# Kernel optimization log

Hardware: AMD Instinct MI355X
Metric: run time of the kernel (lower is better)

Reference implementation:

```python
import jax, jax.numpy as jnp
from jax import lax
import numpy as np

TAG_NAMES = ["O", "B-MAT", "I-MAT", "B-PRO", "I-PRO", "B-APL", "I-APL", "B-SMT", "I-SMT", "B-CMT", "I-CMT", "B-DSC", "I-DSC"]
IMP = -100.0


def _init_crf_params(key):
    # torchcrf initializes uniform(-0.1, 0.1); CRF_NEW then clamps invalid
    # BIO transitions to -100 per define_invalid_crf_transitions/init_crf_transitions.
    K = len(TAG_NAMES)
    k1, k2, k3 = jax.random.split(key, 3)
    start = np.array(jax.random.uniform(k1, (K,), minval=-0.1, maxval=0.1), dtype=np.float32)
    end = np.array(jax.random.uniform(k2, (K,), minval=-0.1, maxval=0.1), dtype=np.float32)
    trans = np.array(jax.random.uniform(k3, (K, K), minval=-0.1, maxval=0.1), dtype=np.float32)
    pref = [t[0] for t in TAG_NAMES]
    ent = [t.split('-')[1] if '-' in t else '' for t in TAG_NAMES]
    for i in range(K):
        if pref[i] in ('B', 'I'):  # invalid begin/end for BIO
            start[i] = IMP
            end[i] = IMP
    for i in range(K):
        for j in range(K):
            # invalid_transitions_position: O -> I  (B->P, I->P are empty sets)
            if pref[i] == 'O' and pref[j] == 'I':
                trans[i, j] = IMP
            # invalid_transitions_tags: B->I, I->I across different entity types
            if pref[i] in ('B', 'I') and pref[j] == 'I' and ent[i] != ent[j]:
                trans[i, j] = IMP
    return jnp.asarray(start), jnp.asarray(end), jnp.asarray(trans)


def setup_inputs() -> dict:
    key = jax.random.key(0)
    k_em, k_tag, k_p = jax.random.split(key, 3)
    B, T, K = 4096, 512, len(TAG_NAMES)
    emissions = jax.random.normal(k_em, (B, T, K), dtype=jnp.float32)
    tags = jax.random.randint(k_tag, (B, T), 0, K, dtype=jnp.int64)
    mask = jnp.ones((B, T), dtype=bool)
    start_transitions, end_transitions, transitions = _init_crf_params(k_p)
    return {"emissions": emissions, "tags": tags, "mask": mask,
            "start_transitions": start_transitions,
            "end_transitions": end_transitions,
            "transitions": transitions}


def reference(emissions, tags, mask, start_transitions, end_transitions, transitions):
    # torchcrf CRF.forward with batch_first=True, reduction='sum':
    # returns sum over batch of log p(tags | emissions).
    B, T, K = emissions.shape
    maskf = mask.astype(emissions.dtype)

    # ---- numerator: score of the given tag path ----
    emit = jnp.take_along_axis(emissions, tags[..., None], axis=2)[..., 0]  # [B,T]
    trans = transitions[tags[:, :-1], tags[:, 1:]]                           # [B,T-1]
    num = start_transitions[tags[:, 0]] + emit[:, 0]
    num = num + jnp.sum((trans + emit[:, 1:]) * maskf[:, 1:], axis=1)
    seq_ends = jnp.sum(mask.astype(jnp.int32), axis=1) - 1                   # [B]
    last_tags = tags[jnp.arange(B), seq_ends]
    num = num + end_transitions[last_tags]

    # ---- denominator: log partition via forward-algorithm scan over time ----
    em_t = jnp.swapaxes(emissions, 0, 1)   # [T,B,K]
    mask_t = jnp.swapaxes(mask, 0, 1)      # [T,B]
    score0 = start_transitions + em_t[0]   # [B,K]

    def step(score, xs):
        em, m = xs  # em: [B,K], m: [B]
        # broadcast: [B,K_from,1] + [K_from,K_to] + [B,1,K_to]
        nxt = jax.nn.logsumexp(score[:, :, None] + transitions[None] + em[:, None, :], axis=1)
        return jnp.where(m[:, None], nxt, score), None

    score, _ = lax.scan(step, score0, (em_t[1:], mask_t[1:]))
    denom = jax.nn.logsumexp(score + end_transitions, axis=1)  # [B]

    return jnp.sum(num - denom)
```

## Files before the change

### kernel.cpp

```cpp
#include <hip/hip_runtime.h>


typedef float  f4  __attribute__((ext_vector_type(4)));
typedef float  f4u __attribute__((ext_vector_type(4), aligned(4)));
typedef int    i4  __attribute__((ext_vector_type(4)));
typedef __bf16 bh8 __attribute__((ext_vector_type(8)));

#define FENCE do { __builtin_amdgcn_sched_barrier(0); \
                   asm volatile("" ::: "memory"); } while (0)

__device__ __forceinline__ unsigned pack_bf16(float x, float y) {
  return __builtin_amdgcn_perm(__float_as_uint(y) + 0x8000u,
                               __float_as_uint(x) + 0x8000u, 0x07060302u);
}

__global__ void __launch_bounds__(192, 1)
crf_main(const float* __restrict__ em,
         const int*   __restrict__ tags,
         const float* __restrict__ startT,
         const float* __restrict__ endT,
         const float* __restrict__ trans,
         float* __restrict__ partial)
{
  __shared__ float ldsT[256];
  __shared__ float ldsS[16], ldsE[16];
  __shared__ float pFa[256];
  __shared__ float lsF[16], numF[16], resB[16];

  const int tid = threadIdx.x;
  for (int i = tid; i < 169; i += 192) {
    const int r_ = i / 13, c_ = i - r_ * 13;
    ldsT[r_ * 16 + c_] = trans[i];
  }
  if (tid < 13) ldsS[tid] = startT[tid];
  if (tid >= 16 && tid < 29) ldsE[tid - 16] = endT[tid - 16];
  __syncthreads();

  const int lane = tid & 63;
  const int wv   = tid >> 6;
  const int n    = lane & 15;
  const int q    = lane >> 4;

  f4  D = {0.f, 0.f, 0.f, 0.f};
  int ls2 = 0;
  float sDs0 = 0, sDs1 = 0, sDs2 = 0, sDs3 = 0;

  if (wv == 2) {
    const int s = q;
    const int seq = blockIdx.x * 16 + n;
    const int* tq = tags + (size_t)seq * 512;
    const float* emQ = em + (size_t)seq * 6656;
    const int t0base = 128 * s;
    float nacc = 0.0f;
    int prev = (s > 0) ? tq[t0base - 1] : 0;
#pragma unroll 4
    for (int g = 0; g < 32; ++g) {
      const int t0 = t0base + 4 * g;
      const int4 tv = *(const int4*)(tq + t0);
      nacc += emQ[(size_t)(t0 + 0) * 13 + tv.x];
      nacc += emQ[(size_t)(t0 + 1) * 13 + tv.y];
      nacc += emQ[(size_t)(t0 + 2) * 13 + tv.z];
      nacc += emQ[(size_t)(t0 + 3) * 13 + tv.w];
      if (!(s == 0 && g == 0)) nacc += ldsT[prev * 16 + tv.x];
      nacc += ldsT[tv.x * 16 + tv.y] + ldsT[tv.y * 16 + tv.z]
            + ldsT[tv.z * 16 + tv.w];
      prev = tv.w;
    }
    if (s == 0) nacc += ldsS[tq[0]];
    if (s == 3) nacc += ldsE[prev];
    nacc += __shfl_xor(nacc, 16, 64);
    nacc += __shfl_xor(nacc, 32, 64);
    if (s == 0) numF[n] = nacc;
  } else {
    const bool is_fwd = (wv == 0);
    const int seq = blockIdx.x * 16 + n;
    const int loadBase = (q < 3) ? 4 * q : 9;
    const float* emP = em + (size_t)seq * 6656 + loadBase;

    bh8 afrag;
    {
      float av[4];
#pragma unroll
      for (int i = 0; i < 4; ++i) {
        const int kk = 4 * q + i;
        av[i] = (kk < 13 && n < 13)
              ? __expf(is_fwd ? ldsT[kk * 16 + n] : ldsT[n * 16 + kk]) : 0.0f;
      }
      i4 ai = { (int)pack_bf16(av[0], av[1]), (int)pack_bf16(av[2], av[3]), 0, 0 };
      afrag = __builtin_bit_cast(bh8, ai);
    }

#pragma unroll
    for (int r = 0; r < 4; ++r) {
      const int m = 4 * q + r;
      D[r] = (m < 13) ? __expf(is_fwd ? ldsS[m] : ldsE[m]) : 0.0f;
    }

    int   epend = 0;
    float rcCur = 1.0f;
    f4 eA[16], eB[16];

#define LOADE(EB, TC) do {                                              \
    const int tc_ = (TC);                                               \
    _Pragma("unroll")                                                   \
    for (int k_ = 0; k_ < 16; ++k_)                                     \
      EB[k_] = *(const f4u*)(emP + (size_t)(tc_ + k_) * 13);            \
  } while (0)

#define RNMEAS() do {                                                   \
    float cm_ = fmaxf(fmaxf(Ds0, Ds1), fmaxf(Ds2, Ds3));                \
    cm_ = fmaxf(cm_, __shfl_xor(cm_, 16, 64));                          \
    cm_ = fmaxf(cm_, __shfl_xor(cm_, 32, 64));                          \
    const int eb_ = (int)(__float_as_uint(cm_) >> 23);                  \
    epend = eb_ - 126;                                                  \
    rcCur = __uint_as_float((unsigned)(253 - eb_) << 23);               \
  } while (0)

#define CORE(EM4, KPH) do {                                             \
    float e0 = __expf((q == 3) ? (EM4).w : (EM4).x);                    \
    float e1 = __expf((EM4).y);                                         \
    float e2 = __expf((EM4).z);                                         \
    float e3 = __expf((EM4).w);                                         \
    if ((KPH) == 7) { e0 *= rcCur; e1 *= rcCur; e2 *= rcCur; e3 *= rcCur; \
                      ls2 += epend; }                                   \
    Ds0 = D[0] * e0; Ds1 = D[1] * e1; Ds2 = D[2] * e2; Ds3 = D[3] * e3; \
    if ((KPH) == 5) RNMEAS();                                           \
    {                                                                   \
      i4 bi_ = { (int)pack_bf16(Ds0, Ds1), (int)pack_bf16(Ds2, Ds3), 0, 0 }; \
      bh8 bf_ = __builtin_bit_cast(bh8, bi_);                           \
      D = __builtin_amdgcn_mfma_f32_16x16x32_bf16(                      \
              afrag, bf_, (f4){0.f, 0.f, 0.f, 0.f}, 0, 0, 0);           \
    }                                                                   \
  } while (0)

#define PROCF(EB, LAST) do {                                            \
    _Pragma("unroll")                                                   \
    for (int k = 0; k < 16; ++k) {                                      \
      const f4 em4 = EB[k];                                             \
      float Ds0, Ds1, Ds2, Ds3;                                         \
      CORE(em4, (k & 7));                                               \
      if ((LAST) && k == 15) { sDs0 = Ds0; sDs1 = Ds1; sDs2 = Ds2; sDs3 = Ds3; } \
    }                                                                   \
  } while (0)

#define PROCB(EB) do {                                                  \
    _Pragma("unroll")                                                   \
    for (int kk = 0; kk < 16; ++kk) {                                   \
      const f4 em4 = EB[15 - kk];                                       \
      float Ds0, Ds1, Ds2, Ds3;                                         \
      CORE(em4, (kk & 7));                                              \
    }                                                                   \
  } while (0)

    if (is_fwd) {
      LOADE(eA, 0); LOADE(eB, 16); FENCE;
      PROCF(eA, false);
      for (int it = 0; it < 7; ++it) {
        LOADE(eA, 32 * it + 32); FENCE;
        PROCF(eB, false);
        LOADE(eB, 32 * it + 48); FENCE;
        PROCF(eA, false);
      }
      FENCE;
      PROCF(eB, true);
      if (q == 0) lsF[n] = (float)ls2 * 0.6931471805599453f;
      *(f4*)&pFa[n * 16 + 4 * q] = (f4){sDs0, sDs1, sDs2, sDs3};
    } else {
      LOADE(eA, 496); LOADE(eB, 480); FENCE;
      PROCB(eA);
      for (int it = 0; it < 7; ++it) {
        LOADE(eA, 464 - 32 * it); FENCE;
        PROCB(eB);
        LOADE(eB, 448 - 32 * it); FENCE;
        PROCB(eA);
      }
      FENCE;
      PROCB(eB);
    }
#undef LOADE
#undef RNMEAS
#undef CORE
#undef PROCF
#undef PROCB
  }

  __syncthreads();

  if (wv == 1) {
    const f4 al = *(const f4*)&pFa[n * 16 + 4 * q];
    float z = al[0] * D[0] + al[1] * D[1] + al[2] * D[2] + al[3] * D[3];
    z += __shfl_xor(z, 16, 64);
    z += __shfl_xor(z, 32, 64);
    const float denom = lsF[n] + (float)ls2 * 0.6931471805599453f + __logf(z);
    if (q == 0) resB[n] = numF[n] - denom;
  }
  __syncthreads();
  if (tid == 0) {
    float s = 0.0f;
#pragma unroll
    for (int i = 0; i < 16; ++i) s += resB[i];
    partial[blockIdx.x] = s;
  }
}

__global__ void __launch_bounds__(256)
crf_reduce(const float* __restrict__ part, float* __restrict__ out, int n)
{
  float v = 0.0f;
  for (int i = threadIdx.x; i < n; i += 256) v += part[i];
#pragma unroll
  for (int off = 32; off > 0; off >>= 1) v += __shfl_down(v, off);
  __shared__ float w[4];
  if ((threadIdx.x & 63) == 0) w[threadIdx.x >> 6] = v;
  __syncthreads();
  if (threadIdx.x == 0) out[0] = (w[0] + w[1]) + (w[2] + w[3]);
}

extern "C" void kernel_launch(void* const* d_in, const int* in_sizes, int n_in,
                              void* d_out, int out_size, void* d_ws, size_t ws_size,
                              hipStream_t stream) {
  const float* em   = (const float*)d_in[0];
  const int*   tags = (const int*)d_in[1];
  const float* st   = (const float*)d_in[3];
  const float* en   = (const float*)d_in[4];
  const float* tr   = (const float*)d_in[5];
  float* part = (float*)d_ws;

  crf_main<<<256, 192, 0, stream>>>(em, tags, st, en, tr, part);
  crf_reduce<<<1, 256, 0, stream>>>(part, (float*)d_out, 256);
}
```

Baseline: 190.8 us.

## Split each sequence's scan into eight parallel chunks of transfer-matrix products

Replaces the two-wave forward/backward scan over 16 sequences per block with one wavefront per sequence. Each wavefront builds eight 13x13 transfer-matrix products over separate time chunks in parallel, using bf16 16x16x16 MFMAs with periodic exponent renormalisation, then chains them with shuffles. The numerator moves to separate blocks and the reduction combines per-sequence numerator and denominator arrays. This adds far more parallel work per sequence to hide the serial MFMA latency of the scan, at the cost of more total MFMA work and more bf16 rounding through the matrix products.

```diff
diff --git a/kernel.cpp b/kernel.cpp
--- a/kernel.cpp
+++ b/kernel.cpp
@@ -2,38 +2,33 @@
 
 
 typedef float  f4  __attribute__((ext_vector_type(4)));
-typedef float  f4u __attribute__((ext_vector_type(4), aligned(4)));
-typedef int    i4  __attribute__((ext_vector_type(4)));
-typedef __bf16 bh8 __attribute__((ext_vector_type(8)));
-
-#define FENCE do { __builtin_amdgcn_sched_barrier(0); \
-                   asm volatile("" ::: "memory"); } while (0)
+typedef short  s4  __attribute__((ext_vector_type(4)));
+typedef int    i2  __attribute__((ext_vector_type(2)));
 
 __device__ __forceinline__ unsigned pack_bf16(float x, float y) {
   return __builtin_amdgcn_perm(__float_as_uint(y) + 0x8000u,
                                __float_as_uint(x) + 0x8000u, 0x07060302u);
 }
 
-__global__ void __launch_bounds__(192, 1)
+__global__ void __launch_bounds__(256)
 crf_main(const float* __restrict__ em,
          const int*   __restrict__ tags,
          const float* __restrict__ startT,
          const float* __restrict__ endT,
          const float* __restrict__ trans,
-         float* __restrict__ partial)
+         float* __restrict__ pnum,
+         float* __restrict__ pden)
 {
   __shared__ float ldsT[256];
   __shared__ float ldsS[16], ldsE[16];
-  __shared__ float pFa[256];
-  __shared__ float lsF[16], numF[16], resB[16];
 
   const int tid = threadIdx.x;
-  for (int i = tid; i < 169; i += 192) {
-    const int r_ = i / 13, c_ = i - r_ * 13;
-    ldsT[r_ * 16 + c_] = trans[i];
-  }
-  if (tid < 13) ldsS[tid] = startT[tid];
-  if (tid >= 16 && tid < 29) ldsE[tid - 16] = endT[tid - 16];
+  for (int i = tid; i < 256; i += 256) {
+    const int r_ = i >> 4, c_ = i & 15;
+    ldsT[i] = (r_ < 13 && c_ < 13) ? trans[r_ * 13 + c_] : -100.0f;
+  }
+  if (tid < 16) ldsS[tid] = (tid < 13) ? startT[tid] : -100.0f;
+  if (tid >= 16 && tid < 32) ldsE[tid - 16] = (tid < 29) ? endT[tid - 16] : -100.0f;
   __syncthreads();
 
   const int lane = tid & 63;
@@ -41,13 +36,9 @@
   const int n    = lane & 15;
   const int q    = lane >> 4;
 
-  f4  D = {0.f, 0.f, 0.f, 0.f};
-  int ls2 = 0;
-  float sDs0 = 0, sDs1 = 0, sDs2 = 0, sDs3 = 0;
-
-  if (wv == 2) {
+  if (blockIdx.x < 64) {
     const int s = q;
-    const int seq = blockIdx.x * 16 + n;
+    const int seq = blockIdx.x * 64 + wv * 16 + n;
     const int* tq = tags + (size_t)seq * 512;
     const float* emQ = em + (size_t)seq * 6656;
     const int t0base = 128 * s;
@@ -70,144 +61,123 @@
     if (s == 3) nacc += ldsE[prev];
     nacc += __shfl_xor(nacc, 16, 64);
     nacc += __shfl_xor(nacc, 32, 64);
-    if (s == 0) numF[n] = nacc;
-  } else {
-    const bool is_fwd = (wv == 0);
-    const int seq = blockIdx.x * 16 + n;
-    const int loadBase = (q < 3) ? 4 * q : 9;
-    const float* emP = em + (size_t)seq * 6656 + loadBase;
-
-    bh8 afrag;
-    {
-      float av[4];
-#pragma unroll
-      for (int i = 0; i < 4; ++i) {
-        const int kk = 4 * q + i;
-        av[i] = (kk < 13 && n < 13)
-              ? __expf(is_fwd ? ldsT[kk * 16 + n] : ldsT[n * 16 + kk]) : 0.0f;
-      }
-      i4 ai = { (int)pack_bf16(av[0], av[1]), (int)pack_bf16(av[2], av[3]), 0, 0 };
-      afrag = __builtin_bit_cast(bh8, ai);
-    }
-
-#pragma unroll
-    for (int r = 0; r < 4; ++r) {
-      const int m = 4 * q + r;
-      D[r] = (m < 13) ? __expf(is_fwd ? ldsS[m] : ldsE[m]) : 0.0f;
-    }
-
-    int   epend = 0;
-    float rcCur = 1.0f;
-    f4 eA[16], eB[16];
-
-#define LOADE(EB, TC) do {                                              \
-    const int tc_ = (TC);                                               \
-    _Pragma("unroll")                                                   \
-    for (int k_ = 0; k_ < 16; ++k_)                                     \
-      EB[k_] = *(const f4u*)(emP + (size_t)(tc_ + k_) * 13);            \
-  } while (0)
-
-#define RNMEAS() do {                                                   \
-    float cm_ = fmaxf(fmaxf(Ds0, Ds1), fmaxf(Ds2, Ds3));                \
-    cm_ = fmaxf(cm_, __shfl_xor(cm_, 16, 64));                          \
-    cm_ = fmaxf(cm_, __shfl_xor(cm_, 32, 64));                          \
-    const int eb_ = (int)(__float_as_uint(cm_) >> 23);                  \
-    epend = eb_ - 126;                                                  \
-    rcCur = __uint_as_float((unsigned)(253 - eb_) << 23);               \
-  } while (0)
-
-#define CORE(EM4, KPH) do {                                             \
-    float e0 = __expf((q == 3) ? (EM4).w : (EM4).x);                    \
-    float e1 = __expf((EM4).y);                                         \
-    float e2 = __expf((EM4).z);                                         \
-    float e3 = __expf((EM4).w);                                         \
-    if ((KPH) == 7) { e0 *= rcCur; e1 *= rcCur; e2 *= rcCur; e3 *= rcCur; \
-                      ls2 += epend; }                                   \
-    Ds0 = D[0] * e0; Ds1 = D[1] * e1; Ds2 = D[2] * e2; Ds3 = D[3] * e3; \
-    if ((KPH) == 5) RNMEAS();                                           \
-    {                                                                   \
-      i4 bi_ = { (int)pack_bf16(Ds0, Ds1), (int)pack_bf16(Ds2, Ds3), 0, 0 }; \
-      bh8 bf_ = __builtin_bit_cast(bh8, bi_);                           \
-      D = __builtin_amdgcn_mfma_f32_16x16x32_bf16(                      \
-              afrag, bf_, (f4){0.f, 0.f, 0.f, 0.f}, 0, 0, 0);           \
+    if (q == 0) pnum[seq] = nacc;
+    return;
+  }
+
+  const int seq = (blockIdx.x - 64) * 4 + wv;
+  const float* emSeq = em + (size_t)seq * 6656;
+  const int mcl = (n < 13) ? n : 0;
+
+  float av[4];
+#pragma unroll
+  for (int i = 0; i < 4; ++i) {
+    const int kk = 4 * q + i;
+    av[i] = (kk < 13 && n < 13) ? __expf(ldsT[kk * 16 + n]) : 0.0f;
+  }
+
+  f4 S[8];
+#pragma unroll
+  for (int j = 0; j < 8; ++j) {
+#pragma unroll
+    for (int r = 0; r < 4; ++r) S[j][r] = (4 * q + r == n) ? 1.0f : 0.0f;
+  }
+
+  float rc[8];
+#pragma unroll
+  for (int j = 0; j < 8; ++j) rc[j] = 1.0f;
+  int ls2 = 0;
+  float eb[8][4];
+  int voff[8];
+
+#pragma unroll
+  for (int j = 0; j < 8; ++j) {
+    const int tb = (j == 0) ? 1 : 64 * j;
+#pragma unroll
+    for (int p = 0; p < 4; ++p)
+      eb[j][(tb + p) & 3] = emSeq[(tb + p) * 13 + mcl];
+    voff[j] = (tb + 4) * 13 + mcl;
+  }
+
+#define STEP(J, RR) do {                                                \
+    const int sl_ = (RR) & 3;                                           \
+    const float ev_ = eb[J][sl_];                                       \
+    eb[J][sl_] = emSeq[voff[J]];                                        \
+    voff[J] = min(voff[J] + 13, 6655);      \
+    float e_ = (n < 13) ? __expf(ev_) : 0.0f;                           \
+    if ((RR) == 7) e_ *= rc[J];               \
+    const unsigned af0_ = pack_bf16(av[0] * e_, av[1] * e_);            \
+    const unsigned af1_ = pack_bf16(av[2] * e_, av[3] * e_);            \
+    const unsigned b0_  = pack_bf16(S[J][0], S[J][1]);                  \
+    const unsigned b1_  = pack_bf16(S[J][2], S[J][3]);                  \
+    i2 ai_ = { (int)af0_, (int)af1_ };                                  \
+    i2 bi_ = { (int)b0_,  (int)b1_  };                                  \
+    S[J] = __builtin_amdgcn_mfma_f32_16x16x16bf16_1k(                   \
+             __builtin_bit_cast(s4, ai_), __builtin_bit_cast(s4, bi_),  \
+             (f4){0.f, 0.f, 0.f, 0.f}, 0, 0, 0);                        \
+    if ((RR) == 5) {                        \
+      float mx_ = fmaxf(fmaxf(S[J][0], S[J][1]), fmaxf(S[J][2], S[J][3])); \
+      mx_ = fmaxf(mx_, __shfl_xor(mx_, 1, 64));                         \
+      mx_ = fmaxf(mx_, __shfl_xor(mx_, 2, 64));                         \
+      mx_ = fmaxf(mx_, __shfl_xor(mx_, 4, 64));                         \
+      mx_ = fmaxf(mx_, __shfl_xor(mx_, 8, 64));                         \
+      mx_ = fmaxf(mx_, __shfl_xor(mx_, 16, 64));                        \
+      mx_ = fmaxf(mx_, __shfl_xor(mx_, 32, 64));                        \
+      const int ebb_ = (int)(__float_as_uint(mx_) >> 23);               \
+      ls2 += ebb_ - 126;                                                \
+      rc[J] = __uint_as_float((unsigned)(253 - ebb_) << 23);            \
     }                                                                   \
   } while (0)
 
-#define PROCF(EB, LAST) do {                                            \
-    _Pragma("unroll")                                                   \
-    for (int k = 0; k < 16; ++k) {                                      \
-      const f4 em4 = EB[k];                                             \
-      float Ds0, Ds1, Ds2, Ds3;                                         \
-      CORE(em4, (k & 7));                                               \
-      if ((LAST) && k == 15) { sDs0 = Ds0; sDs1 = Ds1; sDs2 = Ds2; sDs3 = Ds3; } \
-    }                                                                   \
-  } while (0)
-
-#define PROCB(EB) do {                                                  \
-    _Pragma("unroll")                                                   \
-    for (int kk = 0; kk < 16; ++kk) {                                   \
-      const f4 em4 = EB[15 - kk];                                       \
-      float Ds0, Ds1, Ds2, Ds3;                                         \
-      CORE(em4, (kk & 7));                                              \
-    }                                                                   \
-  } while (0)
-
-    if (is_fwd) {
-      LOADE(eA, 0); LOADE(eB, 16); FENCE;
-      PROCF(eA, false);
-      for (int it = 0; it < 7; ++it) {
-        LOADE(eA, 32 * it + 32); FENCE;
-        PROCF(eB, false);
-        LOADE(eB, 32 * it + 48); FENCE;
-        PROCF(eA, false);
-      }
-      FENCE;
-      PROCF(eB, true);
-      if (q == 0) lsF[n] = (float)ls2 * 0.6931471805599453f;
-      *(f4*)&pFa[n * 16 + 4 * q] = (f4){sDs0, sDs1, sDs2, sDs3};
-    } else {
-      LOADE(eA, 496); LOADE(eB, 480); FENCE;
-      PROCB(eA);
-      for (int it = 0; it < 7; ++it) {
-        LOADE(eA, 464 - 32 * it); FENCE;
-        PROCB(eB);
-        LOADE(eB, 448 - 32 * it); FENCE;
-        PROCB(eA);
-      }
-      FENCE;
-      PROCB(eB);
+#define RND_ALL(RR) do { STEP(0, RR); STEP(1, RR); STEP(2, RR); STEP(3, RR); \
+                         STEP(4, RR); STEP(5, RR); STEP(6, RR); STEP(7, RR); } while (0)
+
+  STEP(1, 0); STEP(2, 0); STEP(3, 0); STEP(4, 0);
+  STEP(5, 0); STEP(6, 0); STEP(7, 0);
+  RND_ALL(1); RND_ALL(2); RND_ALL(3); RND_ALL(4);
+  RND_ALL(5); RND_ALL(6); RND_ALL(7);
+#pragma unroll 1
+  for (int o = 1; o < 8; ++o) {
+    RND_ALL(0); RND_ALL(1); RND_ALL(2); RND_ALL(3);
+    RND_ALL(4); RND_ALL(5); RND_ALL(6); RND_ALL(7);
+  }
+
+  float a_n;
+  {
+    const float em0 = emSeq[mcl];
+    a_n = (n < 13) ? __expf(ldsS[n] + em0) : 0.0f;
+  }
+#pragma unroll
+  for (int s = 0; s < 8; ++s) {
+    float t0 = S[s][0] * a_n, t1 = S[s][1] * a_n,
+          t2 = S[s][2] * a_n, t3 = S[s][3] * a_n;
+#pragma unroll
+    for (int mk = 1; mk <= 8; mk <<= 1) {
+      t0 += __shfl_xor(t0, mk, 64); t1 += __shfl_xor(t1, mk, 64);
+      t2 += __shfl_xor(t2, mk, 64); t3 += __shfl_xor(t3, mk, 64);
     }
-#undef LOADE
-#undef RNMEAS
-#undef CORE
-#undef PROCF
-#undef PROCB
-  }
-
-  __syncthreads();
-
-  if (wv == 1) {
-    const f4 al = *(const f4*)&pFa[n * 16 + 4 * q];
-    float z = al[0] * D[0] + al[1] * D[1] + al[2] * D[2] + al[3] * D[3];
-    z += __shfl_xor(z, 16, 64);
-    z += __shfl_xor(z, 32, 64);
-    const float denom = lsF[n] + (float)ls2 * 0.6931471805599453f + __logf(z);
-    if (q == 0) resB[n] = numF[n] - denom;
-  }
-  __syncthreads();
-  if (tid == 0) {
-    float s = 0.0f;
-#pragma unroll
-    for (int i = 0; i < 16; ++i) s += resB[i];
-    partial[blockIdx.x] = s;
-  }
+    const int srcL = ((n >> 2) << 4) | n;
+    const float b0 = __shfl(t0, srcL, 64), b1 = __shfl(t1, srcL, 64);
+    const float b2 = __shfl(t2, srcL, 64), b3 = __shfl(t3, srcL, 64);
+    const int r2 = n & 3;
+    a_n = (r2 == 0) ? b0 : (r2 == 1) ? b1 : (r2 == 2) ? b2 : b3;
+  }
+  float d = (n < 13) ? a_n * __expf(ldsE[n]) : 0.0f;
+#pragma unroll
+  for (int mk = 1; mk <= 8; mk <<= 1) d += __shfl_xor(d, mk, 64);
+  const float denom = __logf(d) + (float)ls2 * 0.6931471805599453f;
+  if (lane == 0) pden[seq] = denom;
+
+#undef STEP
+#undef RND_ALL
 }
 
 __global__ void __launch_bounds__(256)
-crf_reduce(const float* __restrict__ part, float* __restrict__ out, int n)
+crf_reduce(const float* __restrict__ pn, const float* __restrict__ pd,
+           float* __restrict__ out)
 {
   float v = 0.0f;
-  for (int i = threadIdx.x; i < n; i += 256) v += part[i];
+  for (int i = threadIdx.x; i < 4096; i += 256) v += pn[i] - pd[i];
 #pragma unroll
   for (int off = 32; off > 0; off >>= 1) v += __shfl_down(v, off);
   __shared__ float w[4];
@@ -224,8 +194,9 @@
   const float* st   = (const float*)d_in[3];
   const float* en   = (const float*)d_in[4];
   const float* tr   = (const float*)d_in[5];
-  float* part = (float*)d_ws;
-
-  crf_main<<<256, 192, 0, stream>>>(em, tags, st, en, tr, part);
-  crf_reduce<<<1, 256, 0, stream>>>(part, (float*)d_out, 256);
-}
+  float* pnum = (float*)d_ws;
+  float* pden = pnum + 4096;
+
+  crf_main<<<1088, 256, 0, stream>>>(em, tags, st, en, tr, pnum, pden);
+  crf_reduce<<<1, 256, 0, stream>>>(pnum, pden, (float*)d_out);
+}
```

Measured after the change: 305.8 us. 60.3% more time.
